# Performance work log

Measured on AMD Instinct MI355X. Metric: run time of the kernel, lower is better.

## Reference

```python
import jax, jax.numpy as jnp
import numpy as np

B, T, D, H = 32, 2048, 256, 256


def setup_inputs() -> dict:
    key = jax.random.key(0)
    ks = jax.random.split(key, 7)
    stdv = 1.0 / float(np.sqrt(H))
    u = lambda k, shape: jax.random.uniform(k, shape, jnp.float32, -stdv, stdv)
    return {
        "x": jax.random.normal(ks[0], (B, T, D), jnp.float32),
        # gate order along the 4H axis: i, f, c, o (stacked = same math as 4 separate matmuls)
        "W_f": u(ks[1], (D, 4 * H)),
        "U_f": u(ks[2], (H, 4 * H)),
        "b_f": u(ks[3], (4 * H,)),
        "W_b": u(ks[4], (D, 4 * H)),
        "U_b": u(ks[5], (H, 4 * H)),
        "b_b": u(ks[6], (4 * H,)),
    }


def _bilstm(x, W_f, U_f, b_f, W_b, U_b, b_b):
    Bk = x.shape[0]
    Hh = U_f.shape[0]
    # precompute input projections for all timesteps (one big GEMM per direction)
    xw_f = jnp.einsum('btd,dg->tbg', x, W_f) + b_f            # [T,B,4H]
    xw_b = jnp.einsum('btd,dg->tbg', x[:, ::-1], W_b) + b_b   # time-reversed input
    h0 = jnp.zeros((Bk, Hh), x.dtype)
    carry0 = (h0, h0, h0, h0)  # h, c, h_back, c_back

    def step(carry, inp):
        h, c, hb, cb = carry
        gw, gwb = inp  # [B,4H] each
        # NOTE: original module applies sigmoid to ALL four gates (incl. candidate g)
        g = jax.nn.sigmoid(gw + h @ U_f)
        i, f, gg, o = jnp.split(g, 4, axis=-1)
        c = f + c + i * gg          # faithful: additive forget term
        h = o + jnp.tanh(c)         # faithful: additive output term
        gb = jax.nn.sigmoid(gwb + hb @ U_b)
        ib, fb, ggb, ob = jnp.split(gb, 4, axis=-1)
        cb = fb + cb + ib * ggb
        hb = ob + jnp.tanh(cb)
        return (h, c, hb, cb), (h, hb)

    (h, c, hb, cb), (hs, hbs) = jax.lax.scan(step, carry0, (xw_f, xw_b))
    hs = jnp.transpose(hs, (1, 0, 2))              # [B,T,H]
    hbs = jnp.transpose(hbs, (1, 0, 2))[:, ::-1]   # flip back to forward time order
    y_net = jnp.concatenate([hs, hbs], axis=2)     # [B,T,2H]
    y_t = jnp.concatenate([h, hb], axis=1)         # [B,2H]
    return y_t, y_net


def reference(x, W_f, U_f, b_f, W_b, U_b, b_b):
    return _bilstm(x, W_f, U_f, b_f, W_b, U_b, b_b)
```

## Files before the change

kernel.cpp:

```cpp
#include <hip/hip_runtime.h>
#include <stdint.h>


#define TT 2048

typedef __attribute__((ext_vector_type(8))) short  short8;
typedef __attribute__((ext_vector_type(8))) __bf16 bf16x8;
typedef __attribute__((ext_vector_type(4))) float  f32x4;
typedef __attribute__((ext_vector_type(4))) int    i32x4;
typedef __attribute__((ext_vector_type(4))) uint32_t u32x4;

#define XW_BYTES    (2ull*TT*32*1024*2)
#define STAGE_BYTES (2ull*TT*32*256*2)

__device__ __forceinline__ unsigned short f2bf(float x){
  uint32_t u = __float_as_uint(x);
  return (unsigned short)((u + 0x7fffu + ((u>>16)&1u)) >> 16);
}
__device__ __forceinline__ float bf2f(unsigned short h){
  return __uint_as_float(((uint32_t)h)<<16);
}

__global__ __launch_bounds__(512, 2)
void k_xw(const float* __restrict__ x, const float* __restrict__ Wf,
          const float* __restrict__ Wb, const float* __restrict__ bf,
          const float* __restrict__ bb, uint16_t* __restrict__ xw)
{
  __shared__ uint16_t wt[1024*32];
  const int bid = blockIdx.x;
  const int d   = bid >> 10;
  const int t0  = (bid & 1023) * 2;
  const float* __restrict__ W    = d ? Wb : Wf;
  const float* __restrict__ bias = d ? bb : bf;
  const int tid  = threadIdx.x;
  const int lane = tid & 63;
  const int wv   = tid >> 6;
  const int mt   = wv >> 1;
  const int nh   = wv & 1;
  const int l15  = lane & 15, lg = lane >> 4;

  f32x4 acc[32];
#pragma unroll
  for (int i=0;i<32;i++) acc[i] = (f32x4){0.f,0.f,0.f,0.f};

  const int arow = mt*16 + l15;
  const int ab   = arow & 31;
  const int atl  = arow >> 5;
  const float* __restrict__ xrow = x + ((size_t)ab*TT + (t0+atl))*256;

  for (int kc = 0; kc < 8; ++kc) {
    const int k0 = kc*32;
    __syncthreads();
#pragma unroll
    for (int cc=0; cc<2; ++cc){
      const int c = tid + cc*512;
      union { unsigned short s[32]; short8 v8[4]; } u;
#pragma unroll
      for (int j=0;j<32;j++) u.s[j] = f2bf(W[(size_t)(k0+j)*1024 + c]);
      short8* dst = (short8*)&wt[c*32];
#pragma unroll
      for (int o=0;o<4;o++) dst[o ^ (c&3)] = u.v8[o];
    }
    __syncthreads();
    union { unsigned short s[8]; short8 v; } af;
    {
      const float4 a0 = *(const float4*)&xrow[k0 + lg*8];
      const float4 a1 = *(const float4*)&xrow[k0 + lg*8 + 4];
      af.s[0]=f2bf(a0.x); af.s[1]=f2bf(a0.y); af.s[2]=f2bf(a0.z); af.s[3]=f2bf(a0.w);
      af.s[4]=f2bf(a1.x); af.s[5]=f2bf(a1.y); af.s[6]=f2bf(a1.z); af.s[7]=f2bf(a1.w);
    }
#pragma unroll
    for (int nt=0; nt<32; ++nt){
      const int ct = nh*512 + nt*16 + l15;
      short8 bfr = *(const short8*)&wt[ct*32 + ((lg ^ (ct&3))<<3)];
      acc[nt] = __builtin_amdgcn_mfma_f32_16x16x32_bf16(
        __builtin_bit_cast(bf16x8, af.v), __builtin_bit_cast(bf16x8, bfr), acc[nt], 0,0,0);
    }
  }
#pragma unroll
  for (int nt=0; nt<32; ++nt){
    const int c = nh*512 + nt*16 + l15;
    const int gate = c >> 8, hc = c & 255;
    const float bv = bias[c];
#pragma unroll
    for (int q=0;q<4;q++){
      const int row = mt*16 + lg*4 + q;
      const int b = row & 31, tl = row >> 5;
      xw[((size_t)(d*TT + t0 + tl)*32 + b)*1024 + hc*4 + gate] = f2bf(acc[nt][q] + bv);
    }
  }
}

__global__ __launch_bounds__(512, 1)
void k_rec(const float* __restrict__ Uf, const float* __restrict__ Ub,
           const uint16_t* __restrict__ xw, uint16_t* __restrict__ stage,
           float* __restrict__ out)
{
  const int bid = blockIdx.x;
  const int d   = bid >> 3;
  const int bs  = bid & 7;
  const int tid  = threadIdx.x;
  const int lane = tid & 63;
  const int w    = tid >> 6;
  const int l15  = lane & 15, lg = lane >> 4;

  const float* __restrict__ U = d ? Ub : Uf;

  __shared__ uint32_t preLds[4096];
  __shared__ __align__(16) unsigned char hlds[2][1024];

  i32x4 aU[8][4];
#pragma unroll
  for (int q=0;q<4;q++)
#pragma unroll
    for (int j=0;j<2;j++){
      const int g = q*256 + (w*2+j)*16 + l15;
#pragma unroll
      for (int m=0;m<4;m++){
        uint32_t rg[4] = {0,0,0,0};
#pragma unroll
        for (int jj=0;jj<16;jj++){
          const int k = m*64 + lg*16 + jj;
          float u = U[(size_t)k*1024 + g];
          int v = __float2int_rn(u * 2032.0f);
          v = v > 127 ? 127 : (v < -127 ? -127 : v);
          rg[jj>>2] |= (uint32_t)(v & 255) << ((jj&3)*8);
        }
        aU[q*2+j][m] = (i32x4){(int)rg[0],(int)rg[1],(int)rg[2],(int)rg[3]};
      }
    }

  ((uint32_t*)hlds)[tid < 512 ? tid : 0] = 0u;
  __syncthreads();

  const int cb  = lane & 3;
  const int hx2 = lane >> 2;
  const int gb  = bs*4 + cb;
  const int hc0 = w*32 + hx2*2;
  const int swz = (cb<<1) | (cb>>1);
  i32x4* pre16 = (i32x4*)preLds;
  const int preR = w*128 + cb*32;
  const float DQ = 1.0f / (2032.0f * 63.5f);

  float cs0=0.f, cs1=0.f, h0=0.f, h1=0.f;

  auto gwload = [&](int t)->u32x4 {
    int tt = t < TT ? t : TT-1;
    int tg = d ? (TT-1-tt) : tt;
    return *(const u32x4*)(xw + (((size_t)(d*TT + tg)*32 + gb)<<10) + hc0*4);
  };
  u32x4 gw0 = gwload(0), gw1 = gwload(1);

  for (int t = 0; t < TT; t += 2) {
#pragma unroll
    for (int half = 0; half < 2; ++half) {
      const int tc  = t + half;
      const int pin = half;

      i32x4 acc[8];
#pragma unroll
      for (int i=0;i<8;i++) acc[i] = (i32x4){0,0,0,0};
      {
        const unsigned char* hb = &hlds[pin][cb*256];
#pragma unroll
        for (int m=0;m<4;m++){
          i32x4 hf = *(const i32x4*)(hb + ((m*64 + lg*16) ^ (swz<<4)));
#pragma unroll
          for (int i=0;i<8;i++)
            acc[i] = __builtin_amdgcn_mfma_i32_16x16x64_i8(aU[i][m], hf, acc[i], 0,0,0);
        }
      }
      if (l15 < 4){
        const int pw = w*128 + l15*32;
        const int sz = (l15<<1) | (l15>>1);
#pragma unroll
        for (int j=0;j<2;j++)
#pragma unroll
          for (int r=0;r<4;r++){
            i32x4 v = (i32x4){acc[j][r], acc[2+j][r], acc[4+j][r], acc[6+j][r]};
            pre16[pw + ((j*16 + lg*4 + r) ^ sz)] = v;
          }
      }
      asm volatile("s_waitcnt lgkmcnt(0)" ::: "memory");
      __builtin_amdgcn_sched_barrier(0);

      i32x4 pA = pre16[preR + ((hx2*2)     ^ swz)];
      i32x4 pB = pre16[preR + ((hx2*2 + 1) ^ swz)];
      const u32x4 gwc = half ? gw1 : gw0;
      float prA[4], prB[4];
#pragma unroll
      for (int q=0;q<4;q++){
        prA[q] = (float)pA[q]*DQ + bf2f((unsigned short)(gwc[q>>1]     >> ((q&1)*16)));
        prB[q] = (float)pB[q]*DQ + bf2f((unsigned short)(gwc[2+(q>>1)] >> ((q&1)*16)));
      }
      float si0 = __builtin_amdgcn_rcpf(1.0f + __expf(-prA[0]));
      float sf0 = __builtin_amdgcn_rcpf(1.0f + __expf(-prA[1]));
      float sg0 = __builtin_amdgcn_rcpf(1.0f + __expf(-prA[2]));
      float so0 = __builtin_amdgcn_rcpf(1.0f + __expf(-prA[3]));
      float si1 = __builtin_amdgcn_rcpf(1.0f + __expf(-prB[0]));
      float sf1 = __builtin_amdgcn_rcpf(1.0f + __expf(-prB[1]));
      float sg1 = __builtin_amdgcn_rcpf(1.0f + __expf(-prB[2]));
      float so1 = __builtin_amdgcn_rcpf(1.0f + __expf(-prB[3]));
      cs0 = sf0 + cs0 + si0*sg0;
      cs1 = sf1 + cs1 + si1*sg1;
      float th0 = 1.0f - 2.0f*__builtin_amdgcn_rcpf(1.0f + __expf(2.0f*cs0));
      float th1 = 1.0f - 2.0f*__builtin_amdgcn_rcpf(1.0f + __expf(2.0f*cs1));
      h0 = so0 + th0;
      h1 = so1 + th1;

      int q0 = (int)(h0 * 63.5f + 0.5f); q0 = q0 > 127 ? 127 : q0;
      int q1 = (int)(h1 * 63.5f + 0.5f); q1 = q1 > 127 ? 127 : q1;
      *(uint16_t*)&hlds[pin^1][cb*256 + (hc0 ^ (swz<<4))] = (uint16_t)(q0 | (q1<<8));

      {
        const int tg = d ? (TT-1-tc) : tc;
        *(uint32_t*)&stage[(((size_t)(d*TT + tg)*32 + gb)<<8) + hc0] =
            (uint32_t)f2bf(h0) | ((uint32_t)f2bf(h1) << 16);
      }
      if (half) gw1 = gwload(tc+2); else gw0 = gwload(tc+2);

      asm volatile("s_waitcnt lgkmcnt(0)" ::: "memory");
      __builtin_amdgcn_sched_barrier(0);
      __builtin_amdgcn_s_barrier();
      __builtin_amdgcn_sched_barrier(0);
    }
  }

  float2 yv; yv.x = h0; yv.y = h1;
  *(float2*)&out[(size_t)gb*512 + d*256 + hc0] = yv;
}

__global__ __launch_bounds__(256)
void k_out(const uint16_t* __restrict__ stage, float* __restrict__ y_net)
{
  const int blk = blockIdx.x;
  const int b = blk >> 11;
  const int t = blk & 2047;
  const int tid = threadIdx.x;
  const uint16_t v0 = stage[((size_t)(0*TT + t)*32 + b)*256 + tid];
  const uint16_t v1 = stage[((size_t)(1*TT + t)*32 + b)*256 + tid];
  float* o = y_net + ((size_t)b*TT + t)*512;
  o[tid]       = bf2f(v0);
  o[tid + 256] = bf2f(v1);
}

extern "C" void kernel_launch(void* const* d_in, const int* in_sizes, int n_in,
                              void* d_out, int out_size, void* d_ws, size_t ws_size,
                              hipStream_t stream)
{
  const float* x  = (const float*)d_in[0];
  const float* Wf = (const float*)d_in[1];
  const float* Uf = (const float*)d_in[2];
  const float* bf = (const float*)d_in[3];
  const float* Wb = (const float*)d_in[4];
  const float* Ub = (const float*)d_in[5];
  const float* bb = (const float*)d_in[6];
  float* out = (float*)d_out;
  uint8_t* ws = (uint8_t*)d_ws;
  uint16_t* xw    = (uint16_t*)ws;
  uint16_t* stage = (uint16_t*)(ws + XW_BYTES);

  k_xw <<<dim3(2048),    dim3(512), 0, stream>>>(x, Wf, Wb, bf, bb, xw);
  k_rec<<<dim3(16),      dim3(512), 0, stream>>>(Uf, Ub, xw, stage, out);
  k_out<<<dim3(32*2048), dim3(256), 0, stream>>>(stage, out + 32*512);
}
```

Measured before the change: 2.795 ms.

## Split recurrent kernel across 1024 threads, halving per-wave MFMA and gate work

The recurrent kernel now runs with 16 waves per block instead of 8. Each wave holds half as many quantized U fragments (4 gate tiles instead of 8) and each lane computes one hidden unit instead of two. The LDS pre-activation layout and swizzle are reworked to match. The goal is to shorten the serial per-timestep critical path by spreading MFMA and activation work over more waves. The cost is a barrier across twice as many waves each step and narrower global and LDS stores.

New measurement: 2.704 ms. 1.03x faster.

```diff
diff --git a/kernel.cpp b/kernel.cpp
--- a/kernel.cpp
+++ b/kernel.cpp
@@ -8,7 +8,6 @@
 typedef __attribute__((ext_vector_type(8))) __bf16 bf16x8;
 typedef __attribute__((ext_vector_type(4))) float  f32x4;
 typedef __attribute__((ext_vector_type(4))) int    i32x4;
-typedef __attribute__((ext_vector_type(4))) uint32_t u32x4;
 
 #define XW_BYTES    (2ull*TT*32*1024*2)
 #define STAGE_BYTES (2ull*TT*32*256*2)
@@ -91,7 +90,7 @@
   }
 }
 
-__global__ __launch_bounds__(512, 1)
+__global__ __launch_bounds__(1024)
 void k_rec(const float* __restrict__ Uf, const float* __restrict__ Ub,
            const uint16_t* __restrict__ xw, uint16_t* __restrict__ stage,
            float* __restrict__ out)
@@ -103,53 +102,46 @@
   const int lane = tid & 63;
   const int w    = tid >> 6;
   const int l15  = lane & 15, lg = lane >> 4;
+  const int cb   = lane & 3;
+  const int hx   = lane >> 2;
+  const int gb   = bs*4 + cb;
 
   const float* __restrict__ U = d ? Ub : Uf;
 
-  __shared__ uint32_t preLds[4096];
+  __shared__ i32x4 pre16[16*64];
   __shared__ __align__(16) unsigned char hlds[2][1024];
 
-  i32x4 aU[8][4];
-#pragma unroll
-  for (int q=0;q<4;q++)
-#pragma unroll
-    for (int j=0;j<2;j++){
-      const int g = q*256 + (w*2+j)*16 + l15;
-#pragma unroll
-      for (int m=0;m<4;m++){
-        uint32_t rg[4] = {0,0,0,0};
-#pragma unroll
-        for (int jj=0;jj<16;jj++){
-          const int k = m*64 + lg*16 + jj;
-          float u = U[(size_t)k*1024 + g];
-          int v = __float2int_rn(u * 2032.0f);
-          v = v > 127 ? 127 : (v < -127 ? -127 : v);
-          rg[jj>>2] |= (uint32_t)(v & 255) << ((jj&3)*8);
-        }
-        aU[q*2+j][m] = (i32x4){(int)rg[0],(int)rg[1],(int)rg[2],(int)rg[3]};
-      }
-    }
-
-  ((uint32_t*)hlds)[tid < 512 ? tid : 0] = 0u;
+  i32x4 aU[4][4];
+#pragma unroll
+  for (int q=0;q<4;q++){
+    const int g = q*256 + w*16 + l15;
+#pragma unroll
+    for (int m=0;m<4;m++){
+      uint32_t rg[4] = {0,0,0,0};
+#pragma unroll
+      for (int jj=0;jj<16;jj++){
+        const int k = m*64 + lg*16 + jj;
+        float u = U[(size_t)k*1024 + g];
+        int v = __float2int_rn(u * 2032.0f);
+        v = v > 127 ? 127 : (v < -127 ? -127 : v);
+        rg[jj>>2] |= (uint32_t)(v & 255) << ((jj&3)*8);
+      }
+      aU[q][m] = (i32x4){(int)rg[0],(int)rg[1],(int)rg[2],(int)rg[3]};
+    }
+  }
+
+  ((uint16_t*)hlds)[tid] = 0;
   __syncthreads();
 
-  const int cb  = lane & 3;
-  const int hx2 = lane >> 2;
-  const int gb  = bs*4 + cb;
-  const int hc0 = w*32 + hx2*2;
-  const int swz = (cb<<1) | (cb>>1);
-  i32x4* pre16 = (i32x4*)preLds;
-  const int preR = w*128 + cb*32;
   const float DQ = 1.0f / (2032.0f * 63.5f);
-
-  float cs0=0.f, cs1=0.f, h0=0.f, h1=0.f;
-
-  auto gwload = [&](int t)->u32x4 {
+  float cs = 0.f, hcur = 0.f;
+
+  auto gwload = [&](int t)->uint64_t {
     int tt = t < TT ? t : TT-1;
     int tg = d ? (TT-1-tt) : tt;
-    return *(const u32x4*)(xw + (((size_t)(d*TT + tg)*32 + gb)<<10) + hc0*4);
+    return *(const uint64_t*)(xw + (((size_t)(d*TT + tg)*32 + gb)<<10) + (w*16+hx)*4);
   };
-  u32x4 gw0 = gwload(0), gw1 = gwload(1);
+  uint64_t gw0 = gwload(0), gw1 = gwload(1);
 
   for (int t = 0; t < TT; t += 2) {
 #pragma unroll
@@ -157,65 +149,49 @@
       const int tc  = t + half;
       const int pin = half;
 
-      i32x4 acc[8];
-#pragma unroll
-      for (int i=0;i<8;i++) acc[i] = (i32x4){0,0,0,0};
+      i32x4 acc[4];
+#pragma unroll
+      for (int q=0;q<4;q++) acc[q] = (i32x4){0,0,0,0};
       {
         const unsigned char* hb = &hlds[pin][cb*256];
 #pragma unroll
         for (int m=0;m<4;m++){
-          i32x4 hf = *(const i32x4*)(hb + ((m*64 + lg*16) ^ (swz<<4)));
-#pragma unroll
-          for (int i=0;i<8;i++)
-            acc[i] = __builtin_amdgcn_mfma_i32_16x16x64_i8(aU[i][m], hf, acc[i], 0,0,0);
+          i32x4 hf = *(const i32x4*)(hb + ((m*64 + lg*16) ^ (cb<<4)));
+#pragma unroll
+          for (int q=0;q<4;q++)
+            acc[q] = __builtin_amdgcn_mfma_i32_16x16x64_i8(aU[q][m], hf, acc[q], 0,0,0);
         }
       }
       if (l15 < 4){
-        const int pw = w*128 + l15*32;
-        const int sz = (l15<<1) | (l15>>1);
-#pragma unroll
-        for (int j=0;j<2;j++)
-#pragma unroll
-          for (int r=0;r<4;r++){
-            i32x4 v = (i32x4){acc[j][r], acc[2+j][r], acc[4+j][r], acc[6+j][r]};
-            pre16[pw + ((j*16 + lg*4 + r) ^ sz)] = v;
-          }
+#pragma unroll
+        for (int r=0;r<4;r++){
+          i32x4 v = (i32x4){acc[0][r], acc[1][r], acc[2][r], acc[3][r]};
+          pre16[w*64 + l15*16 + ((lg*4 + r + 2*l15) & 15)] = v;
+        }
       }
       asm volatile("s_waitcnt lgkmcnt(0)" ::: "memory");
       __builtin_amdgcn_sched_barrier(0);
 
-      i32x4 pA = pre16[preR + ((hx2*2)     ^ swz)];
-      i32x4 pB = pre16[preR + ((hx2*2 + 1) ^ swz)];
-      const u32x4 gwc = half ? gw1 : gw0;
-      float prA[4], prB[4];
-#pragma unroll
-      for (int q=0;q<4;q++){
-        prA[q] = (float)pA[q]*DQ + bf2f((unsigned short)(gwc[q>>1]     >> ((q&1)*16)));
-        prB[q] = (float)pB[q]*DQ + bf2f((unsigned short)(gwc[2+(q>>1)] >> ((q&1)*16)));
-      }
-      float si0 = __builtin_amdgcn_rcpf(1.0f + __expf(-prA[0]));
-      float sf0 = __builtin_amdgcn_rcpf(1.0f + __expf(-prA[1]));
-      float sg0 = __builtin_amdgcn_rcpf(1.0f + __expf(-prA[2]));
-      float so0 = __builtin_amdgcn_rcpf(1.0f + __expf(-prA[3]));
-      float si1 = __builtin_amdgcn_rcpf(1.0f + __expf(-prB[0]));
-      float sf1 = __builtin_amdgcn_rcpf(1.0f + __expf(-prB[1]));
-      float sg1 = __builtin_amdgcn_rcpf(1.0f + __expf(-prB[2]));
-      float so1 = __builtin_amdgcn_rcpf(1.0f + __expf(-prB[3]));
-      cs0 = sf0 + cs0 + si0*sg0;
-      cs1 = sf1 + cs1 + si1*sg1;
-      float th0 = 1.0f - 2.0f*__builtin_amdgcn_rcpf(1.0f + __expf(2.0f*cs0));
-      float th1 = 1.0f - 2.0f*__builtin_amdgcn_rcpf(1.0f + __expf(2.0f*cs1));
-      h0 = so0 + th0;
-      h1 = so1 + th1;
-
-      int q0 = (int)(h0 * 63.5f + 0.5f); q0 = q0 > 127 ? 127 : q0;
-      int q1 = (int)(h1 * 63.5f + 0.5f); q1 = q1 > 127 ? 127 : q1;
-      *(uint16_t*)&hlds[pin^1][cb*256 + (hc0 ^ (swz<<4))] = (uint16_t)(q0 | (q1<<8));
+      i32x4 pv = pre16[w*64 + cb*16 + ((hx + 2*cb) & 15)];
+      const uint64_t gwc = half ? gw1 : gw0;
+      float pr[4];
+#pragma unroll
+      for (int q=0;q<4;q++)
+        pr[q] = (float)pv[q]*DQ + bf2f((unsigned short)(gwc >> (q*16)));
+      float si = __builtin_amdgcn_rcpf(1.0f + __expf(-pr[0]));
+      float sf = __builtin_amdgcn_rcpf(1.0f + __expf(-pr[1]));
+      float sg = __builtin_amdgcn_rcpf(1.0f + __expf(-pr[2]));
+      float so = __builtin_amdgcn_rcpf(1.0f + __expf(-pr[3]));
+      cs = sf + cs + si*sg;
+      float th = 1.0f - 2.0f*__builtin_amdgcn_rcpf(1.0f + __expf(2.0f*cs));
+      hcur = so + th;
+
+      int q8 = (int)(hcur * 63.5f + 0.5f); q8 = q8 > 127 ? 127 : q8;
+      hlds[pin^1][cb*256 + ((w*16 + hx) ^ (cb<<4))] = (unsigned char)q8;
 
       {
         const int tg = d ? (TT-1-tc) : tc;
-        *(uint32_t*)&stage[(((size_t)(d*TT + tg)*32 + gb)<<8) + hc0] =
-            (uint32_t)f2bf(h0) | ((uint32_t)f2bf(h1) << 16);
+        stage[(((size_t)(d*TT + tg)*32 + gb)<<8) + w*16 + hx] = f2bf(hcur);
       }
       if (half) gw1 = gwload(tc+2); else gw0 = gwload(tc+2);
 
@@ -226,8 +202,7 @@
     }
   }
 
-  float2 yv; yv.x = h0; yv.y = h1;
-  *(float2*)&out[(size_t)gb*512 + d*256 + hc0] = yv;
+  out[(size_t)gb*512 + d*256 + w*16 + hx] = hcur;
 }
 
 __global__ __launch_bounds__(256)
@@ -260,7 +235,7 @@
   uint16_t* xw    = (uint16_t*)ws;
   uint16_t* stage = (uint16_t*)(ws + XW_BYTES);
 
-  k_xw <<<dim3(2048),    dim3(512), 0, stream>>>(x, Wf, Wb, bf, bb, xw);
-  k_rec<<<dim3(16),      dim3(512), 0, stream>>>(Uf, Ub, xw, stage, out);
-  k_out<<<dim3(32*2048), dim3(256), 0, stream>>>(stage, out + 32*512);
-}
+  k_xw <<<dim3(2048),    dim3(512),  0, stream>>>(x, Wf, Wb, bf, bb, xw);
+  k_rec<<<dim3(16),      dim3(1024), 0, stream>>>(Uf, Ub, xw, stage, out);
+  k_out<<<dim3(32*2048), dim3(256),  0, stream>>>(stage, out + 32*512);
+}
```
